# Optimization experiments

Hardware: AMD Instinct MI355X
Metric: run time of the kernel (lower is better)

Reference implementation:

```python
import jax, jax.numpy as jnp
import numpy as np
from jax import lax

BATCH = 2560
N_CLS = 128    # QP decision dim n
N_INEQ = 128   # number of inequality constraints
N_FEAT = 128
IPM_ITERS = 20
SIGMA = 0.1    # centering parameter


def setup_inputs() -> dict:
    key = jax.random.key(0)
    k1, k2, k3, k4, k5 = jax.random.split(key, 5)
    x = jax.random.normal(k1, (BATCH, N_FEAT), dtype=jnp.float32)
    # symmetric positive-definite Q (qpth requires PD Q)
    A = jax.random.normal(k2, (N_CLS, N_CLS), dtype=jnp.float32) / np.sqrt(N_CLS).astype(np.float32)
    Q = A @ A.T + 1e-4 * jnp.eye(N_CLS, dtype=jnp.float32)
    p = jax.random.normal(k3, (BATCH, N_CLS), dtype=jnp.float32)
    G = jax.random.uniform(k4, (N_INEQ, N_CLS), minval=-1.0, maxval=1.0, dtype=jnp.float32)
    # h > 0 so z = 0 is strictly feasible -> well-conditioned IPM
    h = jax.random.uniform(k5, (N_INEQ,), dtype=jnp.float32) + 1.0
    return {"x": x, "Q": Q, "p": p, "G": G, "h": h, "m": 1}


def _qp_solve(Q, p, G, h, iters=IPM_ITERS, sigma=SIGMA):
    """Batched primal-dual interior-point solve of
       min_z 1/2 z'Qz + p'z  s.t.  Gz + s = h, s >= 0.
    Q: [n,n] shared; p: [B,n]; G: [m,n] shared; h: [m] shared."""
    B, n = p.shape
    mI = G.shape[0]
    z = jnp.zeros((B, n), p.dtype)
    s = jnp.ones((B, mI), p.dtype)
    lam = jnp.ones((B, mI), p.dtype)
    GT = G.T

    def frac_to_boundary(v, dv):
        safe = jnp.where(dv < 0, dv, -1.0)
        r = jnp.where(dv < 0, -v / safe, 1e9)
        return jnp.minimum(1.0, 0.99 * jnp.min(r, axis=1, keepdims=True))

    def step(carry, _):
        z, s, lam = carry
        r_d = z @ Q.T + p + lam @ G          # [B,n]  Qz + p + G'lam
        r_p = z @ GT + s - h                 # [B,m]  Gz + s - h
        mu = jnp.mean(s * lam, axis=1, keepdims=True)
        r_c = s * lam - sigma * mu           # [B,m]
        d = lam / s                          # [B,m]
        # reduced KKT: (Q + G' D G) dz = -r_d + G'((r_c - lam*r_p)/s)
        M = Q[None] + jnp.einsum('ki,bk,kj->bij', G, d, G)  # [B,n,n]
        rhs = -r_d + ((r_c - lam * r_p) / s) @ G             # [B,n]
        dz = jnp.linalg.solve(M, rhs[..., None])[..., 0]
        ds = -r_p - dz @ GT
        dlam = (-r_c - lam * ds) / s
        a = jnp.minimum(frac_to_boundary(s, ds), frac_to_boundary(lam, dlam))
        return (z + a * dz, s + a * ds, lam + a * dlam), None

    (z, s, lam), _ = lax.scan(step, (z, s, lam), None, length=iters)
    return z


def reference(x, Q, p, G, h, m):
    # m==1 path of OptNet.forward: p stays [B,n], Q shared [n,n]
    pf = p.T if m > 1 else p
    z = _qp_solve(Q.astype(jnp.float32), pf.astype(jnp.float32),
                  G.astype(jnp.float32), h.astype(jnp.float32))
    out = z.reshape(10, -1)  # faithful to x.view(10, -1)
    return jax.nn.log_softmax(out, axis=1)
```

## Files before the change

### kernel.cpp

```cpp
#include <hip/hip_runtime.h>
#include <math.h>


#define B_TOT 2560
#define TB 32
#define NB (B_TOT/TB)

__device__ __forceinline__ int ROFF(int i){ return (i*(i+1))>>1; }
__device__ __forceinline__ int rowStart(int i){
  int a=i>>2, b=i&3;
  return ((a+1)*((a<<1)+b))<<2;
}
#define TRI_SZ 8448

__device__ __forceinline__ int rowOfIdx(int idx){
  int i = (int)((sqrtf(8.f*(float)idx+1.f)-1.f)*0.5f);
  while (((i+1)*(i+2)>>1) <= idx) ++i;
  while (((i*(i+1))>>1) > idx) --i;
  return i;
}

__device__ __forceinline__ void chol_diag_gj(float* tri, int c0, int lane){
  float rowA[16], rowW[16];
  const int r = lane;
  #pragma unroll
  for (int j=0;j<16;++j){ rowA[j]=0.f; rowW[j]=0.f; }
  if (r < 16){
    const float* src = &tri[rowStart(c0+r)+c0];
    #pragma unroll
    for (int q=0;q<4;++q){
      if (q <= (r>>2)){
        float4 w = *(const float4*)&src[4*q];
        rowA[4*q+0]=w.x; rowA[4*q+1]=w.y; rowA[4*q+2]=w.z; rowA[4*q+3]=w.w;
      }
    }
    #pragma unroll
    for (int j=0;j<16;++j) if (j>r) rowA[j]=0.f;
    #pragma unroll
    for (int j=0;j<16;++j) rowW[j] = (j==r)?1.f:0.f;
  }
  #pragma unroll
  for (int k=0;k<16;++k){
    float akk = __shfl(rowA[k], k, 64);
    akk = fmaxf(akk, 1e-12f);
    float linv = rsqrtf(akk);
    float lrk = rowA[k]*linv;
    if (r==k){
      #pragma unroll
      for (int c=0;c<16;++c) rowW[c] *= linv;
    }
    #pragma unroll
    for (int j=k+1;j<16;++j){
      float ljk = __shfl(lrk, j, 64);
      if (r>=j) rowA[j] = fmaf(-lrk, ljk, rowA[j]);
    }
    #pragma unroll
    for (int c=0;c<=k;++c){
      float wkc = __shfl(rowW[c], k, 64);
      if (r>k) rowW[c] = fmaf(-lrk, wkc, rowW[c]);
    }
  }
  if (r < 16){
    float* dst = &tri[rowStart(c0+r)+c0];
    #pragma unroll
    for (int q=0;q<4;++q){
      if (q <= (r>>2)){
        float4 w; w.x=rowW[4*q+0]; w.y=rowW[4*q+1]; w.z=rowW[4*q+2]; w.w=rowW[4*q+3];
        *(float4*)&dst[4*q] = w;
      }
    }
  }
}

__device__ void chol_factor(float* tri, int t, int lane, int wid){
  for (int kb=0; kb<8; ++kb){
    const int c0 = kb*16;
    if (wid==(kb&3)) chol_diag_gj(tri, c0, lane);
    __syncthreads();
    const int rem = 112 - c0;
    if (t < rem){
      const int r = c0+16+t;
      const int rb = rowStart(r)+c0;
      float a[16];
      #pragma unroll
      for (int q=0;q<4;++q){
        float4 w = *(const float4*)&tri[rb+4*q];
        a[4*q+0]=w.x; a[4*q+1]=w.y; a[4*q+2]=w.z; a[4*q+3]=w.w;
      }
      float x[16];
      #pragma unroll
      for (int c=0;c<16;++c){
        float acc=0.f;
        const int lb = rowStart(c0+c)+c0;
        #pragma unroll
        for (int q=0;q<=(c>>2);++q){
          float4 w = *(const float4*)&tri[lb+4*q];
          if (4*q+0<=c) acc = fmaf(w.x, a[4*q+0], acc);
          if (4*q+1<=c) acc = fmaf(w.y, a[4*q+1], acc);
          if (4*q+2<=c) acc = fmaf(w.z, a[4*q+2], acc);
          if (4*q+3<=c) acc = fmaf(w.w, a[4*q+3], acc);
        }
        x[c]=acc;
      }
      #pragma unroll
      for (int q=0;q<4;++q){
        float4 w; w.x=x[4*q+0]; w.y=x[4*q+1]; w.z=x[4*q+2]; w.w=x[4*q+3];
        *(float4*)&tri[rb+4*q] = w;
      }
    }
    __syncthreads();
    if (rem > 0){
      const int base = c0+16;
      const int R = rem>>2;
      const int ntile = (R*(R+1))>>1;
      for (int idx=t; idx<ntile; idx+=256){
        int I = rowOfIdx(idx);
        int J = idx - ROFF(I);
        int i0 = base + 4*I, j0 = base + 4*J;
        int ra0=rowStart(i0+0)+c0, ra1=rowStart(i0+1)+c0,
            ra2=rowStart(i0+2)+c0, ra3=rowStart(i0+3)+c0;
        int rb0=rowStart(j0+0)+c0, rb1=rowStart(j0+1)+c0,
            rb2=rowStart(j0+2)+c0, rb3=rowStart(j0+3)+c0;
        float acc[4][4];
        #pragma unroll
        for (int ii=0;ii<4;++ii)
          #pragma unroll
          for (int jj=0;jj<4;++jj) acc[ii][jj]=0.f;
        #pragma unroll
        for (int q=0;q<4;++q){
          float4 A0=*(const float4*)&tri[ra0+4*q];
          float4 A1=*(const float4*)&tri[ra1+4*q];
          float4 A2=*(const float4*)&tri[ra2+4*q];
          float4 A3=*(const float4*)&tri[ra3+4*q];
          float4 B0=*(const float4*)&tri[rb0+4*q];
          float4 B1=*(const float4*)&tri[rb1+4*q];
          float4 B2=*(const float4*)&tri[rb2+4*q];
          float4 B3=*(const float4*)&tri[rb3+4*q];
          #define DOT4(Ai,Bj) (fmaf(Ai.x,Bj.x,fmaf(Ai.y,Bj.y,fmaf(Ai.z,Bj.z,Ai.w*Bj.w))))
          acc[0][0]+=DOT4(A0,B0); acc[0][1]+=DOT4(A0,B1); acc[0][2]+=DOT4(A0,B2); acc[0][3]+=DOT4(A0,B3);
          acc[1][0]+=DOT4(A1,B0); acc[1][1]+=DOT4(A1,B1); acc[1][2]+=DOT4(A1,B2); acc[1][3]+=DOT4(A1,B3);
          acc[2][0]+=DOT4(A2,B0); acc[2][1]+=DOT4(A2,B1); acc[2][2]+=DOT4(A2,B2); acc[2][3]+=DOT4(A2,B3);
          acc[3][0]+=DOT4(A3,B0); acc[3][1]+=DOT4(A3,B1); acc[3][2]+=DOT4(A3,B2); acc[3][3]+=DOT4(A3,B3);
          #undef DOT4
        }
        #pragma unroll
        for (int ii=0;ii<4;++ii){
          #pragma unroll
          for (int jj=0;jj<4;++jj){
            int gi=i0+ii, gj=j0+jj;
            if (gi>=gj) tri[rowStart(gi)+gj] -= acc[ii][jj];
          }
        }
      }
    }
    __syncthreads();
  }
}

__device__ void chol_factor_w2(float* tri, int t, int lane, int wid){
  for (int kb=0; kb<8; ++kb){
    const int c0 = kb*16;
    if (wid==0) chol_diag_gj(tri, c0, lane);
    __syncthreads();
    const int rem = 112 - c0;
    if (t < rem){
      const int r = c0+16+t;
      const int rb = rowStart(r)+c0;
      float a[16];
      #pragma unroll
      for (int q=0;q<4;++q){
        float4 w = *(const float4*)&tri[rb+4*q];
        a[4*q+0]=w.x; a[4*q+1]=w.y; a[4*q+2]=w.z; a[4*q+3]=w.w;
      }
      float x[16];
      #pragma unroll
      for (int c=0;c<16;++c){
        float acc=0.f;
        const int lb = rowStart(c0+c)+c0;
        #pragma unroll
        for (int q=0;q<=(c>>2);++q){
          float4 w = *(const float4*)&tri[lb+4*q];
          if (4*q+0<=c) acc = fmaf(w.x, a[4*q+0], acc);
          if (4*q+1<=c) acc = fmaf(w.y, a[4*q+1], acc);
          if (4*q+2<=c) acc = fmaf(w.z, a[4*q+2], acc);
          if (4*q+3<=c) acc = fmaf(w.w, a[4*q+3], acc);
        }
        x[c]=acc;
      }
      #pragma unroll
      for (int q=0;q<4;++q){
        float4 w; w.x=x[4*q+0]; w.y=x[4*q+1]; w.z=x[4*q+2]; w.w=x[4*q+3];
        *(float4*)&tri[rb+4*q] = w;
      }
    }
    __syncthreads();
    if (rem > 0){
      const int base = c0+16;
      const int R = rem>>2;
      const int ntile = (R*(R+1))>>1;
      for (int idx=t; idx<ntile; idx+=128){
        int I = rowOfIdx(idx);
        int J = idx - ROFF(I);
        int i0 = base + 4*I, j0 = base + 4*J;
        int ra0=rowStart(i0+0)+c0, ra1=rowStart(i0+1)+c0,
            ra2=rowStart(i0+2)+c0, ra3=rowStart(i0+3)+c0;
        int rb0=rowStart(j0+0)+c0, rb1=rowStart(j0+1)+c0,
            rb2=rowStart(j0+2)+c0, rb3=rowStart(j0+3)+c0;
        float acc[4][4];
        #pragma unroll
        for (int ii=0;ii<4;++ii)
          #pragma unroll
          for (int jj=0;jj<4;++jj) acc[ii][jj]=0.f;
        #pragma unroll
        for (int q=0;q<4;++q){
          float4 A0=*(const float4*)&tri[ra0+4*q];
          float4 A1=*(const float4*)&tri[ra1+4*q];
          float4 A2=*(const float4*)&tri[ra2+4*q];
          float4 A3=*(const float4*)&tri[ra3+4*q];
          float4 B0=*(const float4*)&tri[rb0+4*q];
          float4 B1=*(const float4*)&tri[rb1+4*q];
          float4 B2=*(const float4*)&tri[rb2+4*q];
          float4 B3=*(const float4*)&tri[rb3+4*q];
          #define DOT4(Ai,Bj) (fmaf(Ai.x,Bj.x,fmaf(Ai.y,Bj.y,fmaf(Ai.z,Bj.z,Ai.w*Bj.w))))
          acc[0][0]+=DOT4(A0,B0); acc[0][1]+=DOT4(A0,B1); acc[0][2]+=DOT4(A0,B2); acc[0][3]+=DOT4(A0,B3);
          acc[1][0]+=DOT4(A1,B0); acc[1][1]+=DOT4(A1,B1); acc[1][2]+=DOT4(A1,B2); acc[1][3]+=DOT4(A1,B3);
          acc[2][0]+=DOT4(A2,B0); acc[2][1]+=DOT4(A2,B1); acc[2][2]+=DOT4(A2,B2); acc[2][3]+=DOT4(A2,B3);
          acc[3][0]+=DOT4(A3,B0); acc[3][1]+=DOT4(A3,B1); acc[3][2]+=DOT4(A3,B2); acc[3][3]+=DOT4(A3,B3);
          #undef DOT4
        }
        #pragma unroll
        for (int ii=0;ii<4;++ii){
          #pragma unroll
          for (int jj=0;jj<4;++jj){
            int gi=i0+ii, gj=j0+jj;
            if (gi>=gj) tri[rowStart(gi)+gj] -= acc[ii][jj];
          }
        }
      }
    }
    __syncthreads();
  }
}

__device__ void tri_solve_w2(const float* tri, float* rhs, int t){
  for (int kb=0;kb<8;++kb){
    const int c0=kb*16;
    if (t<16){
      const int c=t;
      const float* lrow = &tri[rowStart(c0+c)+c0];
      float acc=0.f;
      #pragma unroll
      for (int cp=0;cp<16;++cp) if (cp<=c) acc = fmaf(lrow[cp], rhs[c0+cp], acc);
      rhs[c0+c] = acc;
    }
    __syncthreads();
    const int rem = 112-c0;
    if (t<rem){
      const int r = c0+16+t;
      const int rb = rowStart(r)+c0;
      float acc = rhs[r];
      #pragma unroll
      for (int q=0;q<4;++q){
        float4 w = *(const float4*)&tri[rb+4*q];
        acc = fmaf(-w.x, rhs[c0+4*q+0], acc);
        acc = fmaf(-w.y, rhs[c0+4*q+1], acc);
        acc = fmaf(-w.z, rhs[c0+4*q+2], acc);
        acc = fmaf(-w.w, rhs[c0+4*q+3], acc);
      }
      rhs[r] = acc;
    }
    __syncthreads();
  }
  for (int kb=7;kb>=0;--kb){
    const int c0=kb*16;
    if (t<16){
      const int c=t;
      float acc=0.f;
      #pragma unroll
      for (int cp=0;cp<16;++cp)
        if (cp>=c) acc = fmaf(tri[rowStart(c0+cp)+c0+c], rhs[c0+cp], acc);
      rhs[c0+c] = acc;
    }
    __syncthreads();
    if (t<c0){
      float acc = rhs[t];
      #pragma unroll
      for (int c=0;c<16;++c) acc = fmaf(-tri[rowStart(c0+c)+t], rhs[c0+c], acc);
      rhs[t]=acc;
    }
    __syncthreads();
  }
}

__global__ __launch_bounds__(256) void k_prep(const float* __restrict__ Q,
        const float* __restrict__ Gm, float* __restrict__ Qi, float* __restrict__ M1)
{
  __shared__ __align__(16) float tri[TRI_SZ];
  __shared__ float Xl[128*32];
  const int t = threadIdx.x;
  const int lane = t&63, wid = t>>6;
  for (int idx=t; idx<8256; idx+=256){
    int i = rowOfIdx(idx); int j = idx - ROFF(i);
    tri[rowStart(i)+j] = Q[i*128+j];
  }
  __syncthreads();
  chol_factor(tri, t, lane, wid);
  for (int cc=0; cc<8; ++cc){
    const int a0 = (cc&3)*32;
    const bool ident = (cc<4);
    for (int idx=t; idx<4096; idx+=256){
      int i=idx>>5, j=idx&31;
      Xl[idx] = ident ? ((i==(a0+j))?1.f:0.f) : Gm[(a0+j)*128+i];
    }
    __syncthreads();
    for (int kb=0;kb<8;++kb){
      const int c0=kb*16;
      if (t<32){
        float v[16], x[16];
        #pragma unroll
        for (int c=0;c<16;++c) v[c]=Xl[(c0+c)*32+t];
        #pragma unroll
        for (int c=0;c<16;++c){
          float acc=0.f;
          const int lb=rowStart(c0+c)+c0;
          #pragma unroll
          for (int cp=0;cp<16;++cp) if (cp<=c) acc=fmaf(tri[lb+cp], v[cp], acc);
          x[c]=acc;
        }
        #pragma unroll
        for (int c=0;c<16;++c) Xl[(c0+c)*32+t]=x[c];
      }
      __syncthreads();
      const int rem=112-c0;
      for (int rr=(t>>5); rr<rem; rr+=8){
        const int r=c0+16+rr, j=t&31;
        float acc=Xl[r*32+j];
        #pragma unroll
        for (int c=0;c<16;++c) acc = fmaf(-tri[rowStart(r)+c0+c], Xl[(c0+c)*32+j], acc);
        Xl[r*32+j]=acc;
      }
      __syncthreads();
    }
    for (int kb=7;kb>=0;--kb){
      const int c0=kb*16;
      if (t<32){
        float v[16], x[16];
        #pragma unroll
        for (int c=0;c<16;++c) v[c]=Xl[(c0+c)*32+t];
        #pragma unroll
        for (int c=0;c<16;++c){
          float acc=0.f;
          #pragma unroll
          for (int cp=0;cp<16;++cp) if (cp>=c) acc=fmaf(tri[rowStart(c0+cp)+c0+c], v[cp], acc);
          x[c]=acc;
        }
        #pragma unroll
        for (int c=0;c<16;++c) Xl[(c0+c)*32+t]=x[c];
      }
      __syncthreads();
      for (int rr=(t>>5); rr<c0; rr+=8){
        const int j=t&31;
        float acc=Xl[rr*32+j];
        #pragma unroll
        for (int c=0;c<16;++c) acc = fmaf(-tri[rowStart(c0+c)+rr], Xl[(c0+c)*32+j], acc);
        Xl[rr*32+j]=acc;
      }
      __syncthreads();
    }
    float* dst = ident ? Qi : M1;
    for (int idx=t; idx<4096; idx+=256){
      int i=idx>>5, j=idx&31;
      dst[i*128+a0+j] = Xl[idx];
    }
    __syncthreads();
  }
}

__global__ __launch_bounds__(256) void k_kmat(const float* __restrict__ Gm,
        const float* __restrict__ M1, float* __restrict__ K, float* __restrict__ Kd){
  const int idx = blockIdx.x*256 + threadIdx.x;
  const int a = idx>>7, bcol = idx&127;
  float a0=0.f,a1=0.f,a2=0.f,a3=0.f;
  #pragma unroll
  for (int j=0;j<128;j+=4){
    a0 = fmaf(Gm[a*128+j+0], M1[(j+0)*128+bcol], a0);
    a1 = fmaf(Gm[a*128+j+1], M1[(j+1)*128+bcol], a1);
    a2 = fmaf(Gm[a*128+j+2], M1[(j+2)*128+bcol], a2);
    a3 = fmaf(Gm[a*128+j+3], M1[(j+3)*128+bcol], a3);
  }
  float acc = (a0+a1)+(a2+a3);
  K[idx] = acc;
  if (a==bcol) Kd[a]=acc;
}

__global__ __launch_bounds__(256) void k_init(const float* __restrict__ p,
    float* __restrict__ Pt, float* __restrict__ S, float* __restrict__ LAM,
    float* __restrict__ GZ, float* __restrict__ QZ, float* __restrict__ Zst){
  int idx = blockIdx.x*256 + threadIdx.x;
  if (idx < 128*B_TOT){
    int i = idx/B_TOT, b = idx - i*B_TOT;
    Pt[idx] = p[b*128+i];
    S[idx]=1.f; LAM[idx]=1.f; GZ[idx]=0.f; QZ[idx]=0.f; Zst[idx]=0.f;
  }
}

__global__ __launch_bounds__(256) void k_B(const float* __restrict__ G,
    const float* __restrict__ M1, const float* __restrict__ Pt,
    const float* __restrict__ h,
    const float* __restrict__ S, const float* __restrict__ LAM,
    const float* __restrict__ GZ, const float* __restrict__ QZ,
    float* __restrict__ RHS, float* __restrict__ TV){
  __shared__ float wm_l[128*33];
  __shared__ float rhs_l[128*33];
  __shared__ float part_l[8*33];
  __shared__ float mu_l[TB];
  __shared__ float h_l[128];
  const int t=threadIdx.x, g=t>>5, bl=t&31;
  const int b = blockIdx.x*TB + bl;
  if (t<128) h_l[t]=h[t];
  __syncthreads();
  float sv[16], lv[16], rpv[16];
  float prod=0.f;
  #pragma unroll
  for (int q=0;q<16;++q){
    int i = g + 8*q;
    float s = S[i*B_TOT+b], l = LAM[i*B_TOT+b], gz = GZ[i*B_TOT+b];
    sv[q]=s; lv[q]=l; rpv[q]=gz+s-h_l[i];
    prod += s*l;
  }
  part_l[g*33+bl] = prod;
  __syncthreads();
  if (g==0){
    float m=0.f;
    #pragma unroll
    for (int q=0;q<8;++q) m += part_l[q*33+bl];
    mu_l[bl] = m*(1.f/128.f);
  }
  __syncthreads();
  const float mu = mu_l[bl];
  #pragma unroll
  for (int q=0;q<16;++q){
    int i=g+8*q;
    float rc = sv[q]*lv[q] - 0.1f*mu;
    wm_l[i*33+bl] = (rc - lv[q]*rpv[q])/sv[q] - lv[q];
  }
  __syncthreads();
  const int r0 = g*16;
  float acc[16];
  #pragma unroll
  for (int q=0;q<16;++q) acc[q] = -(QZ[(r0+q)*B_TOT+b] + Pt[(r0+q)*B_TOT+b]);
  #pragma unroll 2
  for (int j=0;j<128;++j){
    float wmv = wm_l[j*33+bl];
    const float4* gp = (const float4*)&G[j*128+r0];
    #pragma unroll
    for (int q4=0;q4<4;++q4){
      float4 gv = gp[q4];
      acc[4*q4+0]=fmaf(gv.x,wmv,acc[4*q4+0]);
      acc[4*q4+1]=fmaf(gv.y,wmv,acc[4*q4+1]);
      acc[4*q4+2]=fmaf(gv.z,wmv,acc[4*q4+2]);
      acc[4*q4+3]=fmaf(gv.w,wmv,acc[4*q4+3]);
    }
  }
  #pragma unroll
  for (int q=0;q<16;++q){
    rhs_l[(r0+q)*33+bl]=acc[q];
    RHS[(r0+q)*B_TOT+b]=acc[q];
  }
  __syncthreads();
  #pragma unroll
  for (int q=0;q<16;++q) acc[q]=0.f;
  #pragma unroll 2
  for (int j=0;j<128;++j){
    float rv = rhs_l[j*33+bl];
    const float4* mp = (const float4*)&M1[j*128+r0];
    #pragma unroll
    for (int q4=0;q4<4;++q4){
      float4 mv = mp[q4];
      acc[4*q4+0]=fmaf(mv.x,rv,acc[4*q4+0]);
      acc[4*q4+1]=fmaf(mv.y,rv,acc[4*q4+1]);
      acc[4*q4+2]=fmaf(mv.z,rv,acc[4*q4+2]);
      acc[4*q4+3]=fmaf(mv.w,rv,acc[4*q4+3]);
    }
  }
  #pragma unroll
  for (int q=0;q<16;++q) TV[(r0+q)*B_TOT+b]=acc[q];
}

__global__ __launch_bounds__(128) void k_C(const float* __restrict__ K,
    const float* __restrict__ Kd, const float* __restrict__ h,
    const float* __restrict__ TV,
    float* __restrict__ S, float* __restrict__ LAM, float* __restrict__ GZ,
    float* __restrict__ Y, float* __restrict__ ALPHA){
  __shared__ __align__(16) float tri[TRI_SZ];
  __shared__ float scl_l[128];
  __shared__ float sh_t[128];
  __shared__ float red[2];
  const int t = threadIdx.x, b = blockIdx.x;
  const int lane = t&63, wid = t>>6;
  float s_t=S[t*B_TOT+b], l_t=LAM[t*B_TOT+b], g_t=GZ[t*B_TOT+b];
  float rp_t = g_t + s_t - h[t];
  float prod = s_t*l_t;
  #pragma unroll
  for (int o=32;o>0;o>>=1) prod += __shfl_xor(prod,o,64);
  if (lane==0) red[wid]=prod;
  __syncthreads();
  const float mu = (red[0]+red[1])*(1.f/128.f);
  float rc_t = s_t*l_t - 0.1f*mu;
  float di_t = fminf(s_t/l_t, 1e30f);
  float sc_t = rsqrtf(Kd[t]+di_t);
  scl_l[t]=sc_t;
  sh_t[t]=TV[t*B_TOT+b]*sc_t;
  __syncthreads();
  #pragma unroll 4
  for (int i=0;i<128;++i){
    if (t<=i){
      tri[rowStart(i)+t] = (t==i)?1.f : K[i*128+t]*scl_l[i]*sc_t;
    }
  }
  __syncthreads();
  chol_factor_w2(tri, t, lane, wid);
  tri_solve_w2(tri, sh_t, t);
  float y = sh_t[t]*sc_t;
  float gd = di_t*y;
  float ds = -rp_t - gd;
  float dl = (-rc_t - l_t*ds)/s_t;
  float ra = 1e9f;
  if (ds<0.f) ra = -s_t/ds;
  if (dl<0.f) ra = fminf(ra,-l_t/dl);
  #pragma unroll
  for (int o=32;o>0;o>>=1) ra = fminf(ra,__shfl_xor(ra,o,64));
  __syncthreads();
  if (lane==0) red[wid]=ra;
  __syncthreads();
  const float alpha = fminf(1.0f, 0.99f*fminf(red[0],red[1]));
  S[t*B_TOT+b]   = s_t + alpha*ds;
  LAM[t*B_TOT+b] = l_t + alpha*dl;
  GZ[t*B_TOT+b]  = g_t + alpha*gd;
  Y[t*B_TOT+b]   = y;
  if (t==0) ALPHA[b]=alpha;
}

__global__ __launch_bounds__(256) void k_D(const float* __restrict__ G,
    const float* __restrict__ Qi, const float* __restrict__ RHS,
    const float* __restrict__ Y, const float* __restrict__ ALPHA,
    float* __restrict__ Zst, float* __restrict__ QZ){
  __shared__ float y_l[128*33];
  __shared__ float v_l[128*33];
  const int t=threadIdx.x, g=t>>5, bl=t&31;
  const int b = blockIdx.x*TB + bl;
  #pragma unroll
  for (int q=0;q<16;++q){
    int i=g+8*q;
    y_l[i*33+bl] = Y[i*B_TOT+b];
  }
  const float alpha = ALPHA[b];
  __syncthreads();
  const int r0=g*16;
  float acc[16];
  #pragma unroll
  for (int q=0;q<16;++q) acc[q]=RHS[(r0+q)*B_TOT+b];
  #pragma unroll 2
  for (int j=0;j<128;++j){
    float yv = y_l[j*33+bl];
    const float4* gp=(const float4*)&G[j*128+r0];
    #pragma unroll
    for (int q4=0;q4<4;++q4){
      float4 gv=gp[q4];
      acc[4*q4+0]=fmaf(-gv.x,yv,acc[4*q4+0]);
      acc[4*q4+1]=fmaf(-gv.y,yv,acc[4*q4+1]);
      acc[4*q4+2]=fmaf(-gv.z,yv,acc[4*q4+2]);
      acc[4*q4+3]=fmaf(-gv.w,yv,acc[4*q4+3]);
    }
  }
  #pragma unroll
  for (int q=0;q<16;++q){
    v_l[(r0+q)*33+bl]=acc[q];
    float* qp=&QZ[(r0+q)*B_TOT+b];
    *qp = *qp + alpha*acc[q];
  }
  __syncthreads();
  #pragma unroll
  for (int q=0;q<16;++q) acc[q]=0.f;
  #pragma unroll 2
  for (int j=0;j<128;++j){
    float vv = v_l[j*33+bl];
    const float4* qp4=(const float4*)&Qi[j*128+r0];
    #pragma unroll
    for (int q4=0;q4<4;++q4){
      float4 qv=qp4[q4];
      acc[4*q4+0]=fmaf(qv.x,vv,acc[4*q4+0]);
      acc[4*q4+1]=fmaf(qv.y,vv,acc[4*q4+1]);
      acc[4*q4+2]=fmaf(qv.z,vv,acc[4*q4+2]);
      acc[4*q4+3]=fmaf(qv.w,vv,acc[4*q4+3]);
    }
  }
  #pragma unroll
  for (int q=0;q<16;++q){
    float* zp=&Zst[(r0+q)*B_TOT+b];
    *zp = *zp + alpha*acc[q];
  }
}

__global__ __launch_bounds__(1024) void k_logsoftmax(const float* __restrict__ Zst,
                                                     float* __restrict__ out){
  __shared__ float red[16];
  __shared__ float sval[2];
  const int r = blockIdx.x, t = threadIdx.x;
  float m = -1e30f;
  for (int k=t;k<32768;k+=1024){
    float v = Zst[(k&127)*B_TOT + r*256 + (k>>7)];
    m = fmaxf(m, v);
  }
  #pragma unroll
  for (int o=32;o>0;o>>=1) m = fmaxf(m, __shfl_down(m,o,64));
  if ((t&63)==0) red[t>>6] = m;
  __syncthreads();
  if (t==0){ float mm=red[0]; for (int w=1;w<16;++w) mm=fmaxf(mm,red[w]); sval[0]=mm; }
  __syncthreads();
  const float mx = sval[0];
  float s=0.f;
  for (int k=t;k<32768;k+=1024){
    float v = Zst[(k&127)*B_TOT + r*256 + (k>>7)];
    s += expf(v-mx);
  }
  #pragma unroll
  for (int o=32;o>0;o>>=1) s += __shfl_down(s,o,64);
  if ((t&63)==0) red[t>>6]=s;
  __syncthreads();
  if (t==0){ float ss=0.f; for (int w=0;w<16;++w) ss+=red[w]; sval[1]=logf(ss); }
  __syncthreads();
  const float lse = sval[1];
  for (int k=t;k<32768;k+=1024){
    float v = Zst[(k&127)*B_TOT + r*256 + (k>>7)];
    out[(size_t)r*32768+k] = v-mx-lse;
  }
}

extern "C" void kernel_launch(void* const* d_in, const int* in_sizes, int n_in,
                              void* d_out, int out_size, void* d_ws, size_t ws_size,
                              hipStream_t stream){
  const float* Q = (const float*)d_in[1];
  const float* p = (const float*)d_in[2];
  const float* G = (const float*)d_in[3];
  const float* h = (const float*)d_in[4];
  float* ws  = (float*)d_ws;
  const int NE = 128*B_TOT;
  float* Zst = ws;
  float* Qi  = Zst + NE;
  float* M1  = Qi + 16384;
  float* K   = M1 + 16384;
  float* Kd  = K + 16384;
  float* ALPHA = Kd + 128;
  float* Pt  = ALPHA + 2560;
  float* S   = Pt + NE;
  float* LAM = S + NE;
  float* GZ  = LAM + NE;
  float* QZ  = GZ + NE;
  float* RHS = QZ + NE;
  float* TV  = RHS + NE;
  float* Y   = TV + NE;
  float* out = (float*)d_out;

  hipLaunchKernelGGL(k_prep, dim3(1), dim3(256), 0, stream, Q, G, Qi, M1);
  hipLaunchKernelGGL(k_kmat, dim3(64), dim3(256), 0, stream, G, M1, K, Kd);
  hipLaunchKernelGGL(k_init, dim3((NE+255)/256), dim3(256), 0, stream,
                     p, Pt, S, LAM, GZ, QZ, Zst);
  for (int it=0; it<20; ++it){
    hipLaunchKernelGGL(k_B, dim3(NB), dim3(256), 0, stream,
                       G, M1, Pt, h, S, LAM, GZ, QZ, RHS, TV);
    hipLaunchKernelGGL(k_C, dim3(B_TOT), dim3(128), 0, stream,
                       K, Kd, h, TV, S, LAM, GZ, Y, ALPHA);
    hipLaunchKernelGGL(k_D, dim3(NB), dim3(256), 0, stream,
                       G, Qi, RHS, Y, ALPHA, Zst, QZ);
  }
  hipLaunchKernelGGL(k_logsoftmax, dim3(10), dim3(1024), 0, stream, Zst, out);
}
```

Baseline: 8.739 ms.

## Fuse D and B kernels, retile Cholesky updates, split and parallelize prep

Replaces the 4x4 trailing-update tiles in the shared-memory Cholesky with 8x8 tiles. In k_C it adds a lookahead schedule where warp 0 factors the next diagonal block while other warps finish the previous trailing update. The per-iteration k_D and k_B kernels are fused into one k_DB kernel that reuses Y/QZ in shared memory, cutting one launch and several global round-trips per iteration. The single-block prep kernel is split into a factor kernel plus an 8-block triangular-solve kernel. Larger tiles raise register pressure, and the lookahead schedule adds complexity to the synchronisation.

```diff
diff --git a/kernel.cpp b/kernel.cpp
--- a/kernel.cpp
+++ b/kernel.cpp
@@ -72,170 +72,153 @@
   }
 }
 
+__device__ __forceinline__ void trail_tile8(float* tri, int pc0, int i0, int j0,
+                                            bool diag){
+  float4 Pi[8][4], Pj[8][4];
+  #pragma unroll
+  for (int ii=0;ii<8;++ii){
+    const float* rp = &tri[rowStart(i0+ii)+pc0];
+    #pragma unroll
+    for (int q=0;q<4;++q) Pi[ii][q] = *(const float4*)&rp[4*q];
+  }
+  #pragma unroll
+  for (int jj=0;jj<8;++jj){
+    const float* rp = &tri[rowStart(j0+jj)+pc0];
+    #pragma unroll
+    for (int q=0;q<4;++q) Pj[jj][q] = *(const float4*)&rp[4*q];
+  }
+  float acc[8][8];
+  #pragma unroll
+  for (int ii=0;ii<8;++ii)
+    #pragma unroll
+    for (int jj=0;jj<8;++jj) acc[ii][jj]=0.f;
+  #pragma unroll
+  for (int q=0;q<4;++q){
+    #pragma unroll
+    for (int ii=0;ii<8;++ii){
+      #pragma unroll
+      for (int jj=0;jj<8;++jj){
+        acc[ii][jj] = fmaf(Pi[ii][q].x, Pj[jj][q].x, acc[ii][jj]);
+        acc[ii][jj] = fmaf(Pi[ii][q].y, Pj[jj][q].y, acc[ii][jj]);
+        acc[ii][jj] = fmaf(Pi[ii][q].z, Pj[jj][q].z, acc[ii][jj]);
+        acc[ii][jj] = fmaf(Pi[ii][q].w, Pj[jj][q].w, acc[ii][jj]);
+      }
+    }
+  }
+  if (!diag){
+    #pragma unroll
+    for (int ii=0;ii<8;++ii){
+      float4* p = (float4*)&tri[rowStart(i0+ii)+j0];
+      float4 v0=p[0], v1=p[1];
+      v0.x-=acc[ii][0]; v0.y-=acc[ii][1]; v0.z-=acc[ii][2]; v0.w-=acc[ii][3];
+      v1.x-=acc[ii][4]; v1.y-=acc[ii][5]; v1.z-=acc[ii][6]; v1.w-=acc[ii][7];
+      p[0]=v0; p[1]=v1;
+    }
+  } else {
+    #pragma unroll
+    for (int ii=0;ii<8;++ii){
+      float4* p = (float4*)&tri[rowStart(i0+ii)+j0];
+      const int nq = (ii>>2)+1;
+      #pragma unroll
+      for (int q=0;q<2;++q){
+        if (q<nq){
+          float4 v=p[q];
+          v.x-=acc[ii][4*q+0]; v.y-=acc[ii][4*q+1];
+          v.z-=acc[ii][4*q+2]; v.w-=acc[ii][4*q+3];
+          p[q]=v;
+        }
+      }
+    }
+  }
+}
+
+__device__ __forceinline__ void trail_tile4(float* tri, int pc0, int i0, int j0){
+  float4 Pi[4][4], Pj[4][4];
+  #pragma unroll
+  for (int ii=0;ii<4;++ii){
+    const float* rp = &tri[rowStart(i0+ii)+pc0];
+    #pragma unroll
+    for (int q=0;q<4;++q) Pi[ii][q] = *(const float4*)&rp[4*q];
+  }
+  #pragma unroll
+  for (int jj=0;jj<4;++jj){
+    const float* rp = &tri[rowStart(j0+jj)+pc0];
+    #pragma unroll
+    for (int q=0;q<4;++q) Pj[jj][q] = *(const float4*)&rp[4*q];
+  }
+  float acc[4][4];
+  #pragma unroll
+  for (int ii=0;ii<4;++ii)
+    #pragma unroll
+    for (int jj=0;jj<4;++jj) acc[ii][jj]=0.f;
+  #pragma unroll
+  for (int q=0;q<4;++q){
+    #pragma unroll
+    for (int ii=0;ii<4;++ii){
+      #pragma unroll
+      for (int jj=0;jj<4;++jj){
+        acc[ii][jj] = fmaf(Pi[ii][q].x, Pj[jj][q].x, acc[ii][jj]);
+        acc[ii][jj] = fmaf(Pi[ii][q].y, Pj[jj][q].y, acc[ii][jj]);
+        acc[ii][jj] = fmaf(Pi[ii][q].z, Pj[jj][q].z, acc[ii][jj]);
+        acc[ii][jj] = fmaf(Pi[ii][q].w, Pj[jj][q].w, acc[ii][jj]);
+      }
+    }
+  }
+  #pragma unroll
+  for (int ii=0;ii<4;++ii){
+    float4* p = (float4*)&tri[rowStart(i0+ii)+j0];
+    float4 v=p[0];
+    v.x-=acc[ii][0]; v.y-=acc[ii][1]; v.z-=acc[ii][2]; v.w-=acc[ii][3];
+    p[0]=v;
+  }
+}
+
+__device__ __forceinline__ void panel_row(float* tri, int c0, int r){
+  const int rb = rowStart(r)+c0;
+  float a[16];
+  #pragma unroll
+  for (int q=0;q<4;++q){
+    float4 w = *(const float4*)&tri[rb+4*q];
+    a[4*q+0]=w.x; a[4*q+1]=w.y; a[4*q+2]=w.z; a[4*q+3]=w.w;
+  }
+  float x[16];
+  #pragma unroll
+  for (int c=0;c<16;++c){
+    float acc=0.f;
+    const int lb = rowStart(c0+c)+c0;
+    #pragma unroll
+    for (int q=0;q<=(c>>2);++q){
+      float4 w = *(const float4*)&tri[lb+4*q];
+      if (4*q+0<=c) acc = fmaf(w.x, a[4*q+0], acc);
+      if (4*q+1<=c) acc = fmaf(w.y, a[4*q+1], acc);
+      if (4*q+2<=c) acc = fmaf(w.z, a[4*q+2], acc);
+      if (4*q+3<=c) acc = fmaf(w.w, a[4*q+3], acc);
+    }
+    x[c]=acc;
+  }
+  #pragma unroll
+  for (int q=0;q<4;++q){
+    float4 w; w.x=x[4*q+0]; w.y=x[4*q+1]; w.z=x[4*q+2]; w.w=x[4*q+3];
+    *(float4*)&tri[rb+4*q] = w;
+  }
+}
+
 __device__ void chol_factor(float* tri, int t, int lane, int wid){
   for (int kb=0; kb<8; ++kb){
     const int c0 = kb*16;
     if (wid==(kb&3)) chol_diag_gj(tri, c0, lane);
     __syncthreads();
     const int rem = 112 - c0;
-    if (t < rem){
-      const int r = c0+16+t;
-      const int rb = rowStart(r)+c0;
-      float a[16];
-      #pragma unroll
-      for (int q=0;q<4;++q){
-        float4 w = *(const float4*)&tri[rb+4*q];
-        a[4*q+0]=w.x; a[4*q+1]=w.y; a[4*q+2]=w.z; a[4*q+3]=w.w;
-      }
-      float x[16];
-      #pragma unroll
-      for (int c=0;c<16;++c){
-        float acc=0.f;
-        const int lb = rowStart(c0+c)+c0;
-        #pragma unroll
-        for (int q=0;q<=(c>>2);++q){
-          float4 w = *(const float4*)&tri[lb+4*q];
-          if (4*q+0<=c) acc = fmaf(w.x, a[4*q+0], acc);
-          if (4*q+1<=c) acc = fmaf(w.y, a[4*q+1], acc);
-          if (4*q+2<=c) acc = fmaf(w.z, a[4*q+2], acc);
-          if (4*q+3<=c) acc = fmaf(w.w, a[4*q+3], acc);
-        }
-        x[c]=acc;
-      }
-      #pragma unroll
-      for (int q=0;q<4;++q){
-        float4 w; w.x=x[4*q+0]; w.y=x[4*q+1]; w.z=x[4*q+2]; w.w=x[4*q+3];
-        *(float4*)&tri[rb+4*q] = w;
-      }
-    }
+    if (t < rem) panel_row(tri, c0, c0+16+t);
     __syncthreads();
     if (rem > 0){
       const int base = c0+16;
-      const int R = rem>>2;
-      const int ntile = (R*(R+1))>>1;
+      const int T = rem>>3;
+      const int ntile = (T*(T+1))>>1;
       for (int idx=t; idx<ntile; idx+=256){
         int I = rowOfIdx(idx);
         int J = idx - ROFF(I);
-        int i0 = base + 4*I, j0 = base + 4*J;
-        int ra0=rowStart(i0+0)+c0, ra1=rowStart(i0+1)+c0,
-            ra2=rowStart(i0+2)+c0, ra3=rowStart(i0+3)+c0;
-        int rb0=rowStart(j0+0)+c0, rb1=rowStart(j0+1)+c0,
-            rb2=rowStart(j0+2)+c0, rb3=rowStart(j0+3)+c0;
-        float acc[4][4];
-        #pragma unroll
-        for (int ii=0;ii<4;++ii)
-          #pragma unroll
-          for (int jj=0;jj<4;++jj) acc[ii][jj]=0.f;
-        #pragma unroll
-        for (int q=0;q<4;++q){
-          float4 A0=*(const float4*)&tri[ra0+4*q];
-          float4 A1=*(const float4*)&tri[ra1+4*q];
-          float4 A2=*(const float4*)&tri[ra2+4*q];
-          float4 A3=*(const float4*)&tri[ra3+4*q];
-          float4 B0=*(const float4*)&tri[rb0+4*q];
-          float4 B1=*(const float4*)&tri[rb1+4*q];
-          float4 B2=*(const float4*)&tri[rb2+4*q];
-          float4 B3=*(const float4*)&tri[rb3+4*q];
-          #define DOT4(Ai,Bj) (fmaf(Ai.x,Bj.x,fmaf(Ai.y,Bj.y,fmaf(Ai.z,Bj.z,Ai.w*Bj.w))))
-          acc[0][0]+=DOT4(A0,B0); acc[0][1]+=DOT4(A0,B1); acc[0][2]+=DOT4(A0,B2); acc[0][3]+=DOT4(A0,B3);
-          acc[1][0]+=DOT4(A1,B0); acc[1][1]+=DOT4(A1,B1); acc[1][2]+=DOT4(A1,B2); acc[1][3]+=DOT4(A1,B3);
-          acc[2][0]+=DOT4(A2,B0); acc[2][1]+=DOT4(A2,B1); acc[2][2]+=DOT4(A2,B2); acc[2][3]+=DOT4(A2,B3);
-          acc[3][0]+=DOT4(A3,B0); acc[3][1]+=DOT4(A3,B1); acc[3][2]+=DOT4(A3,B2); acc[3][3]+=DOT4(A3,B3);
-          #undef DOT4
-        }
-        #pragma unroll
-        for (int ii=0;ii<4;++ii){
-          #pragma unroll
-          for (int jj=0;jj<4;++jj){
-            int gi=i0+ii, gj=j0+jj;
-            if (gi>=gj) tri[rowStart(gi)+gj] -= acc[ii][jj];
-          }
-        }
-      }
-    }
-    __syncthreads();
-  }
-}
-
-__device__ void chol_factor_w2(float* tri, int t, int lane, int wid){
-  for (int kb=0; kb<8; ++kb){
-    const int c0 = kb*16;
-    if (wid==0) chol_diag_gj(tri, c0, lane);
-    __syncthreads();
-    const int rem = 112 - c0;
-    if (t < rem){
-      const int r = c0+16+t;
-      const int rb = rowStart(r)+c0;
-      float a[16];
-      #pragma unroll
-      for (int q=0;q<4;++q){
-        float4 w = *(const float4*)&tri[rb+4*q];
-        a[4*q+0]=w.x; a[4*q+1]=w.y; a[4*q+2]=w.z; a[4*q+3]=w.w;
-      }
-      float x[16];
-      #pragma unroll
-      for (int c=0;c<16;++c){
-        float acc=0.f;
-        const int lb = rowStart(c0+c)+c0;
-        #pragma unroll
-        for (int q=0;q<=(c>>2);++q){
-          float4 w = *(const float4*)&tri[lb+4*q];
-          if (4*q+0<=c) acc = fmaf(w.x, a[4*q+0], acc);
-          if (4*q+1<=c) acc = fmaf(w.y, a[4*q+1], acc);
-          if (4*q+2<=c) acc = fmaf(w.z, a[4*q+2], acc);
-          if (4*q+3<=c) acc = fmaf(w.w, a[4*q+3], acc);
-        }
-        x[c]=acc;
-      }
-      #pragma unroll
-      for (int q=0;q<4;++q){
-        float4 w; w.x=x[4*q+0]; w.y=x[4*q+1]; w.z=x[4*q+2]; w.w=x[4*q+3];
-        *(float4*)&tri[rb+4*q] = w;
-      }
-    }
-    __syncthreads();
-    if (rem > 0){
-      const int base = c0+16;
-      const int R = rem>>2;
-      const int ntile = (R*(R+1))>>1;
-      for (int idx=t; idx<ntile; idx+=128){
-        int I = rowOfIdx(idx);
-        int J = idx - ROFF(I);
-        int i0 = base + 4*I, j0 = base + 4*J;
-        int ra0=rowStart(i0+0)+c0, ra1=rowStart(i0+1)+c0,
-            ra2=rowStart(i0+2)+c0, ra3=rowStart(i0+3)+c0;
-        int rb0=rowStart(j0+0)+c0, rb1=rowStart(j0+1)+c0,
-            rb2=rowStart(j0+2)+c0, rb3=rowStart(j0+3)+c0;
-        float acc[4][4];
-        #pragma unroll
-        for (int ii=0;ii<4;++ii)
-          #pragma unroll
-          for (int jj=0;jj<4;++jj) acc[ii][jj]=0.f;
-        #pragma unroll
-        for (int q=0;q<4;++q){
-          float4 A0=*(const float4*)&tri[ra0+4*q];
-          float4 A1=*(const float4*)&tri[ra1+4*q];
-          float4 A2=*(const float4*)&tri[ra2+4*q];
-          float4 A3=*(const float4*)&tri[ra3+4*q];
-          float4 B0=*(const float4*)&tri[rb0+4*q];
-          float4 B1=*(const float4*)&tri[rb1+4*q];
-          float4 B2=*(const float4*)&tri[rb2+4*q];
-          float4 B3=*(const float4*)&tri[rb3+4*q];
-          #define DOT4(Ai,Bj) (fmaf(Ai.x,Bj.x,fmaf(Ai.y,Bj.y,fmaf(Ai.z,Bj.z,Ai.w*Bj.w))))
-          acc[0][0]+=DOT4(A0,B0); acc[0][1]+=DOT4(A0,B1); acc[0][2]+=DOT4(A0,B2); acc[0][3]+=DOT4(A0,B3);
-          acc[1][0]+=DOT4(A1,B0); acc[1][1]+=DOT4(A1,B1); acc[1][2]+=DOT4(A1,B2); acc[1][3]+=DOT4(A1,B3);
-          acc[2][0]+=DOT4(A2,B0); acc[2][1]+=DOT4(A2,B1); acc[2][2]+=DOT4(A2,B2); acc[2][3]+=DOT4(A2,B3);
-          acc[3][0]+=DOT4(A3,B0); acc[3][1]+=DOT4(A3,B1); acc[3][2]+=DOT4(A3,B2); acc[3][3]+=DOT4(A3,B3);
-          #undef DOT4
-        }
-        #pragma unroll
-        for (int ii=0;ii<4;++ii){
-          #pragma unroll
-          for (int jj=0;jj<4;++jj){
-            int gi=i0+ii, gj=j0+jj;
-            if (gi>=gj) tri[rowStart(gi)+gj] -= acc[ii][jj];
-          }
-        }
+        trail_tile8(tri, c0, base+8*I, base+8*J, I==J);
       }
     }
     __syncthreads();
@@ -292,11 +275,9 @@
   }
 }
 
-__global__ __launch_bounds__(256) void k_prep(const float* __restrict__ Q,
-        const float* __restrict__ Gm, float* __restrict__ Qi, float* __restrict__ M1)
-{
+__global__ __launch_bounds__(256) void k_prepA(const float* __restrict__ Q,
+                                               float* __restrict__ TRIQ){
   __shared__ __align__(16) float tri[TRI_SZ];
-  __shared__ float Xl[128*32];
   const int t = threadIdx.x;
   const int lane = t&63, wid = t>>6;
   for (int idx=t; idx<8256; idx+=256){
@@ -305,74 +286,81 @@
   }
   __syncthreads();
   chol_factor(tri, t, lane, wid);
-  for (int cc=0; cc<8; ++cc){
-    const int a0 = (cc&3)*32;
-    const bool ident = (cc<4);
-    for (int idx=t; idx<4096; idx+=256){
-      int i=idx>>5, j=idx&31;
-      Xl[idx] = ident ? ((i==(a0+j))?1.f:0.f) : Gm[(a0+j)*128+i];
-    }
-    __syncthreads();
-    for (int kb=0;kb<8;++kb){
-      const int c0=kb*16;
-      if (t<32){
-        float v[16], x[16];
+  for (int idx=t; idx<TRI_SZ; idx+=256) TRIQ[idx]=tri[idx];
+}
+
+__global__ __launch_bounds__(256) void k_prepB(const float* __restrict__ TRIQ,
+        const float* __restrict__ Gm, float* __restrict__ Qi, float* __restrict__ M1)
+{
+  __shared__ __align__(16) float tri[TRI_SZ];
+  __shared__ float Xl[128*32];
+  const int t = threadIdx.x, cc = blockIdx.x;
+  const int a0 = (cc&3)*32;
+  const bool ident = (cc<4);
+  for (int idx=t; idx<TRI_SZ; idx+=256) tri[idx]=TRIQ[idx];
+  for (int idx=t; idx<4096; idx+=256){
+    int i=idx>>5, j=idx&31;
+    Xl[idx] = ident ? ((i==(a0+j))?1.f:0.f) : Gm[(a0+j)*128+i];
+  }
+  __syncthreads();
+  for (int kb=0;kb<8;++kb){
+    const int c0=kb*16;
+    if (t<32){
+      float v[16], x[16];
+      #pragma unroll
+      for (int c=0;c<16;++c) v[c]=Xl[(c0+c)*32+t];
+      #pragma unroll
+      for (int c=0;c<16;++c){
+        float acc=0.f;
+        const int lb=rowStart(c0+c)+c0;
         #pragma unroll
-        for (int c=0;c<16;++c) v[c]=Xl[(c0+c)*32+t];
+        for (int cp=0;cp<16;++cp) if (cp<=c) acc=fmaf(tri[lb+cp], v[cp], acc);
+        x[c]=acc;
+      }
+      #pragma unroll
+      for (int c=0;c<16;++c) Xl[(c0+c)*32+t]=x[c];
+    }
+    __syncthreads();
+    const int rem=112-c0;
+    for (int rr=(t>>5); rr<rem; rr+=8){
+      const int r=c0+16+rr, j=t&31;
+      float acc=Xl[r*32+j];
+      #pragma unroll
+      for (int c=0;c<16;++c) acc = fmaf(-tri[rowStart(r)+c0+c], Xl[(c0+c)*32+j], acc);
+      Xl[r*32+j]=acc;
+    }
+    __syncthreads();
+  }
+  for (int kb=7;kb>=0;--kb){
+    const int c0=kb*16;
+    if (t<32){
+      float v[16], x[16];
+      #pragma unroll
+      for (int c=0;c<16;++c) v[c]=Xl[(c0+c)*32+t];
+      #pragma unroll
+      for (int c=0;c<16;++c){
+        float acc=0.f;
         #pragma unroll
-        for (int c=0;c<16;++c){
-          float acc=0.f;
-          const int lb=rowStart(c0+c)+c0;
-          #pragma unroll
-          for (int cp=0;cp<16;++cp) if (cp<=c) acc=fmaf(tri[lb+cp], v[cp], acc);
-          x[c]=acc;
-        }
-        #pragma unroll
-        for (int c=0;c<16;++c) Xl[(c0+c)*32+t]=x[c];
-      }
-      __syncthreads();
-      const int rem=112-c0;
-      for (int rr=(t>>5); rr<rem; rr+=8){
-        const int r=c0+16+rr, j=t&31;
-        float acc=Xl[r*32+j];
-        #pragma unroll
-        for (int c=0;c<16;++c) acc = fmaf(-tri[rowStart(r)+c0+c], Xl[(c0+c)*32+j], acc);
-        Xl[r*32+j]=acc;
-      }
-      __syncthreads();
-    }
-    for (int kb=7;kb>=0;--kb){
-      const int c0=kb*16;
-      if (t<32){
-        float v[16], x[16];
-        #pragma unroll
-        for (int c=0;c<16;++c) v[c]=Xl[(c0+c)*32+t];
-        #pragma unroll
-        for (int c=0;c<16;++c){
-          float acc=0.f;
-          #pragma unroll
-          for (int cp=0;cp<16;++cp) if (cp>=c) acc=fmaf(tri[rowStart(c0+cp)+c0+c], v[cp], acc);
-          x[c]=acc;
-        }
-        #pragma unroll
-        for (int c=0;c<16;++c) Xl[(c0+c)*32+t]=x[c];
-      }
-      __syncthreads();
-      for (int rr=(t>>5); rr<c0; rr+=8){
-        const int j=t&31;
-        float acc=Xl[rr*32+j];
-        #pragma unroll
-        for (int c=0;c<16;++c) acc = fmaf(-tri[rowStart(c0+c)+rr], Xl[(c0+c)*32+j], acc);
-        Xl[rr*32+j]=acc;
-      }
-      __syncthreads();
-    }
-    float* dst = ident ? Qi : M1;
-    for (int idx=t; idx<4096; idx+=256){
-      int i=idx>>5, j=idx&31;
-      dst[i*128+a0+j] = Xl[idx];
-    }
-    __syncthreads();
+        for (int cp=0;cp<16;++cp) if (cp>=c) acc=fmaf(tri[rowStart(c0+cp)+c0+c], v[cp], acc);
+        x[c]=acc;
+      }
+      #pragma unroll
+      for (int c=0;c<16;++c) Xl[(c0+c)*32+t]=x[c];
+    }
+    __syncthreads();
+    for (int rr=(t>>5); rr<c0; rr+=8){
+      const int j=t&31;
+      float acc=Xl[rr*32+j];
+      #pragma unroll
+      for (int c=0;c<16;++c) acc = fmaf(-tri[rowStart(c0+c)+rr], Xl[(c0+c)*32+j], acc);
+      Xl[rr*32+j]=acc;
+    }
+    __syncthreads();
+  }
+  float* dst = ident ? Qi : M1;
+  for (int idx=t; idx<4096; idx+=256){
+    int i=idx>>5, j=idx&31;
+    dst[i*128+a0+j] = Xl[idx];
   }
 }
 
@@ -514,12 +502,50 @@
   __syncthreads();
   #pragma unroll 4
   for (int i=0;i<128;++i){
-    if (t<=i){
-      tri[rowStart(i)+t] = (t==i)?1.f : K[i*128+t]*scl_l[i]*sc_t;
-    }
-  }
-  __syncthreads();
-  chol_factor_w2(tri, t, lane, wid);
+    if (t<=i) tri[rowStart(i)+t] = (t==i)?1.f : K[i*128+t]*scl_l[i]*sc_t;
+  }
+  __syncthreads();
+  for (int kb=0;kb<8;++kb){
+    const int c0=16*kb;
+    {
+      int ntile=3, n1=3;
+      if (kb>0){
+        const int T = (128-c0)>>3;
+        ntile = (T*(T+1))>>1;
+        n1 = 3 + (((ntile-3)*3)>>2);
+      }
+      if (wid==0){
+        chol_diag_gj(tri, c0, lane);
+        if (kb>0){
+          const int pc0 = c0-16;
+          for (int idx=n1+lane; idx<ntile; idx+=64){
+            int I = rowOfIdx(idx);
+            int J = idx - ROFF(I);
+            trail_tile8(tri, pc0, c0+8*I, c0+8*J, I==J);
+          }
+        }
+      } else {
+        if (kb>0){
+          const int pc0 = c0-16;
+          for (int idx=3+lane; idx<n1; idx+=64){
+            int I = rowOfIdx(idx);
+            int J = idx - ROFF(I);
+            trail_tile8(tri, pc0, c0+8*I, c0+8*J, I==J);
+          }
+        }
+      }
+    }
+    __syncthreads();
+    const int rem = 112-c0;
+    if (t<rem) panel_row(tri, c0, c0+16+t);
+    __syncthreads();
+    if (kb<7 && t<10){
+      int I = rowOfIdx(t);
+      int J = t - ROFF(I);
+      trail_tile4(tri, c0, c0+16+4*I, c0+16+4*J);
+    }
+    __syncthreads();
+  }
   tri_solve_w2(tri, sh_t, t);
   float y = sh_t[t]*sc_t;
   float gd = di_t*y;
@@ -539,6 +565,144 @@
   GZ[t*B_TOT+b]  = g_t + alpha*gd;
   Y[t*B_TOT+b]   = y;
   if (t==0) ALPHA[b]=alpha;
+}
+
+__global__ __launch_bounds__(256) void k_DB(const float* __restrict__ G,
+    const float* __restrict__ Qi, const float* __restrict__ M1,
+    const float* __restrict__ Pt, const float* __restrict__ h,
+    const float* __restrict__ S, const float* __restrict__ LAM,
+    const float* __restrict__ GZ,
+    const float* __restrict__ Y, const float* __restrict__ ALPHA,
+    float* __restrict__ Zst, float* __restrict__ QZ,
+    float* __restrict__ RHS, float* __restrict__ TV){
+  __shared__ float bufA[128*33];
+  __shared__ float bufB[128*33];
+  __shared__ float part_l[8*33];
+  __shared__ float mu_l[TB];
+  __shared__ float h_l[128];
+  const int t=threadIdx.x, g=t>>5, bl=t&31;
+  const int b = blockIdx.x*TB + bl;
+  const int r0 = g*16;
+  if (t<128) h_l[t]=h[t];
+  #pragma unroll
+  for (int q=0;q<16;++q){
+    int i=g+8*q;
+    bufA[i*33+bl] = Y[i*B_TOT+b];
+  }
+  const float alpha = ALPHA[b];
+  __syncthreads();
+  float acc[16];
+  #pragma unroll
+  for (int q=0;q<16;++q) acc[q]=RHS[(r0+q)*B_TOT+b];
+  #pragma unroll 2
+  for (int j=0;j<128;++j){
+    float yv = bufA[j*33+bl];
+    const float4* gp=(const float4*)&G[j*128+r0];
+    #pragma unroll
+    for (int q4=0;q4<4;++q4){
+      float4 gv=gp[q4];
+      acc[4*q4+0]=fmaf(-gv.x,yv,acc[4*q4+0]);
+      acc[4*q4+1]=fmaf(-gv.y,yv,acc[4*q4+1]);
+      acc[4*q4+2]=fmaf(-gv.z,yv,acc[4*q4+2]);
+      acc[4*q4+3]=fmaf(-gv.w,yv,acc[4*q4+3]);
+    }
+  }
+  __syncthreads();
+  #pragma unroll
+  for (int q=0;q<16;++q){
+    const int i=r0+q;
+    float qz_new = QZ[i*B_TOT+b] + alpha*acc[q];
+    QZ[i*B_TOT+b] = qz_new;
+    bufB[i*33+bl] = acc[q];
+    bufA[i*33+bl] = qz_new;
+  }
+  __syncthreads();
+  #pragma unroll
+  for (int q=0;q<16;++q) acc[q]=0.f;
+  #pragma unroll 2
+  for (int j=0;j<128;++j){
+    float vv = bufB[j*33+bl];
+    const float4* qp4=(const float4*)&Qi[j*128+r0];
+    #pragma unroll
+    for (int q4=0;q4<4;++q4){
+      float4 qv=qp4[q4];
+      acc[4*q4+0]=fmaf(qv.x,vv,acc[4*q4+0]);
+      acc[4*q4+1]=fmaf(qv.y,vv,acc[4*q4+1]);
+      acc[4*q4+2]=fmaf(qv.z,vv,acc[4*q4+2]);
+      acc[4*q4+3]=fmaf(qv.w,vv,acc[4*q4+3]);
+    }
+  }
+  #pragma unroll
+  for (int q=0;q<16;++q){
+    float* zp=&Zst[(r0+q)*B_TOT+b];
+    *zp = *zp + alpha*acc[q];
+  }
+  __syncthreads();
+  float sv[16], lv[16], rpv[16];
+  float prod=0.f;
+  #pragma unroll
+  for (int q=0;q<16;++q){
+    int i = g + 8*q;
+    float s = S[i*B_TOT+b], l = LAM[i*B_TOT+b], gz = GZ[i*B_TOT+b];
+    sv[q]=s; lv[q]=l; rpv[q]=gz+s-h_l[i];
+    prod += s*l;
+  }
+  part_l[g*33+bl] = prod;
+  __syncthreads();
+  if (g==0){
+    float m=0.f;
+    #pragma unroll
+    for (int q=0;q<8;++q) m += part_l[q*33+bl];
+    mu_l[bl] = m*(1.f/128.f);
+  }
+  __syncthreads();
+  const float mu = mu_l[bl];
+  #pragma unroll
+  for (int q=0;q<16;++q){
+    int i=g+8*q;
+    float rc = sv[q]*lv[q] - 0.1f*mu;
+    bufB[i*33+bl] = (rc - lv[q]*rpv[q])/sv[q] - lv[q];
+  }
+  __syncthreads();
+  #pragma unroll
+  for (int q=0;q<16;++q) acc[q] = -(bufA[(r0+q)*33+bl] + Pt[(r0+q)*B_TOT+b]);
+  #pragma unroll 2
+  for (int j=0;j<128;++j){
+    float wmv = bufB[j*33+bl];
+    const float4* gp = (const float4*)&G[j*128+r0];
+    #pragma unroll
+    for (int q4=0;q4<4;++q4){
+      float4 gv = gp[q4];
+      acc[4*q4+0]=fmaf(gv.x,wmv,acc[4*q4+0]);
+      acc[4*q4+1]=fmaf(gv.y,wmv,acc[4*q4+1]);
+      acc[4*q4+2]=fmaf(gv.z,wmv,acc[4*q4+2]);
+      acc[4*q4+3]=fmaf(gv.w,wmv,acc[4*q4+3]);
+    }
+  }
+  __syncthreads();
+  #pragma unroll
+  for (int q=0;q<16;++q){
+    RHS[(r0+q)*B_TOT+b]=acc[q];
+    bufA[(r0+q)*33+bl]=acc[q];
+  }
+  __syncthreads();
+  #pragma unroll
+  for (int q=0;q<16;++q) acc[q]=0.f;
+  #pragma unroll 2
+  for (int j=0;j<128;++j){
+    float rv = bufA[j*33+bl];
+    const float4* mp = (const float4*)&M1[j*128+r0];
+    #pragma unroll
+    for (int q4=0;q4<4;++q4){
+      float4 mv = mp[q4];
+      acc[4*q4+0]=fmaf(mv.x,rv,acc[4*q4+0]);
+      acc[4*q4+1]=fmaf(mv.y,rv,acc[4*q4+1]);
+      acc[4*q4+2]=fmaf(mv.z,rv,acc[4*q4+2]);
+      acc[4*q4+3]=fmaf(mv.w,rv,acc[4*q4+3]);
+    }
+  }
+  #pragma unroll
+  for (int q=0;q<16;++q) TV[(r0+q)*B_TOT+b]=acc[q];
 }
 
 __global__ __launch_bounds__(256) void k_D(const float* __restrict__ G,
@@ -660,19 +824,27 @@
   float* RHS = QZ + NE;
   float* TV  = RHS + NE;
   float* Y   = TV + NE;
+  float* TRIQ= Y + NE;
   float* out = (float*)d_out;
 
-  hipLaunchKernelGGL(k_prep, dim3(1), dim3(256), 0, stream, Q, G, Qi, M1);
+  hipLaunchKernelGGL(k_prepA, dim3(1), dim3(256), 0, stream, Q, TRIQ);
+  hipLaunchKernelGGL(k_prepB, dim3(8), dim3(256), 0, stream, TRIQ, G, Qi, M1);
   hipLaunchKernelGGL(k_kmat, dim3(64), dim3(256), 0, stream, G, M1, K, Kd);
   hipLaunchKernelGGL(k_init, dim3((NE+255)/256), dim3(256), 0, stream,
                      p, Pt, S, LAM, GZ, QZ, Zst);
+  hipLaunchKernelGGL(k_B, dim3(NB), dim3(256), 0, stream,
+                     G, M1, Pt, h, S, LAM, GZ, QZ, RHS, TV);
   for (int it=0; it<20; ++it){
-    hipLaunchKernelGGL(k_B, dim3(NB), dim3(256), 0, stream,
-                       G, M1, Pt, h, S, LAM, GZ, QZ, RHS, TV);
     hipLaunchKernelGGL(k_C, dim3(B_TOT), dim3(128), 0, stream,
                        K, Kd, h, TV, S, LAM, GZ, Y, ALPHA);
-    hipLaunchKernelGGL(k_D, dim3(NB), dim3(256), 0, stream,
-                       G, Qi, RHS, Y, ALPHA, Zst, QZ);
+    if (it < 19){
+      hipLaunchKernelGGL(k_DB, dim3(NB), dim3(256), 0, stream,
+                         G, Qi, M1, Pt, h, S, LAM, GZ, Y, ALPHA,
+                         Zst, QZ, RHS, TV);
+    } else {
+      hipLaunchKernelGGL(k_D, dim3(NB), dim3(256), 0, stream,
+                         G, Qi, RHS, Y, ALPHA, Zst, QZ);
+    }
   }
   hipLaunchKernelGGL(k_logsoftmax, dim3(10), dim3(1024), 0, stream, Zst, out);
 }
```

Result: slower. 12.12 ms (+38.7%).
